# Kernel optimization log

Hardware: AMD Instinct MI355X
Metric: run time of the kernel (lower is better)

Reference implementation:

```python
import jax, jax.numpy as jnp
import numpy as np

RADIUS = 9.0   # search_raduis_scale * particle_radius
K = 20         # N_neighbor
HIDDEN = [512, 512, 512, 512]


def embed(x, n_freqs):
    freqs = 2.0 ** jnp.arange(n_freqs, dtype=x.dtype)      # [F]
    xf = x[..., None, :] * freqs[:, None]                  # [..., F, C]
    sc = jnp.stack([jnp.sin(xf), jnp.cos(xf)], axis=-2)    # [..., F, 2, C]
    return jnp.concatenate([x, sc.reshape(*x.shape[:-1], -1)], axis=-1)


def ball_query(q, p, radius, k):
    # pytorch3d semantics: first k points (by index order) with squared dist < radius^2;
    # padding slots get dists=0, idx=-1, nn=0.
    n = p.shape[0]
    d2 = jnp.sum((q[:, None, :] - p[None, :, :]) ** 2, axis=-1)   # [P,N]
    valid = d2 < radius * radius
    score = jnp.where(valid, -jnp.arange(n, dtype=q.dtype), -jnp.inf)
    top, idx = jax.lax.top_k(score, k)                            # first k valid indices
    found = top > -jnp.inf
    safe = jnp.clip(idx, 0, n - 1)
    dists = jnp.where(found, jnp.take_along_axis(d2, safe, axis=1), 0.0)
    nn = jnp.where(found[..., None], p[safe], 0.0)                # [P,K,3]
    return dists, jnp.where(found, idx, -1), nn


def mlp(x, params):
    n = len(params)
    for l, (v, g, b) in enumerate(params):
        w = g * v / jnp.linalg.norm(v, axis=1, keepdims=True)     # weight_norm, dim=0
        x = x @ w.T + b
        if l < n - 1:
            x = jax.nn.relu(x)
    return jax.nn.sigmoid(x)


def setup_inputs() -> dict:
    key = jax.random.key(0)
    ks = jax.random.split(key, 32)
    R, S, N, F = 256, 128, 4096, 256
    P = R * S
    inp = {
        "points": jax.random.normal(ks[0], (P, 3), dtype=jnp.float32) * 3.0,
        "normals": jax.random.normal(ks[1], (P, 3), dtype=jnp.float32),
        "view_dirs": jax.random.normal(ks[2], (P, 3), dtype=jnp.float32),
        "feature_vectors": jax.random.normal(ks[3], (P, F), dtype=jnp.float32),
        "phys_points": jax.random.normal(ks[4], (N, 3), dtype=jnp.float32) * 3.0,
        "ray_dirs": jax.random.normal(ks[5], (R, 3), dtype=jnp.float32),
        "cam_loc": jax.random.normal(ks[6], (1, 3), dtype=jnp.float32),
    }
    d0 = 3 + 3 + 3 + F + 63 + 9 + 63 + 63 + 27 + 27   # = 517
    dims = [d0] + HIDDEN + [3]
    for l in range(len(dims) - 1):
        fan_in, fan_out = dims[l], dims[l + 1]
        inp[f"v{l}"] = jax.random.normal(ks[7 + l], (fan_out, fan_in), dtype=jnp.float32) * float(np.sqrt(2.0 / fan_out))
        inp[f"g{l}"] = jnp.ones((fan_out, 1), dtype=jnp.float32)
        inp[f"b{l}"] = jnp.zeros((fan_out,), dtype=jnp.float32)
    return inp


def reference(points, normals, view_dirs, feature_vectors, phys_points, ray_dirs, cam_loc,
              v0, g0, b0, v1, g1, b1, v2, g2, b2, v3, g3, b3, v4, g4, b4):
    params = [(v0, g0, b0), (v1, g1, b1), (v2, g2, b2), (v3, g3, b3), (v4, g4, b4)]
    # mode == 'idr'
    rendering_input = jnp.concatenate([points, view_dirs, normals, feature_vectors], axis=-1)
    dists, idx, neighbors = ball_query(points, phys_points, RADIUS, K)
    nn_mask = dists != 0                                             # [P,K]
    num_nn = nn_mask.sum(-1, keepdims=True).astype(points.dtype)     # [P,1]
    # smoothing_position (exclude_ray=True): Euclidean dists recomputed incl. zero-padded slots
    dd = jnp.linalg.norm(neighbors - points[:, None, :], axis=-1)    # [P,K]
    w = jnp.maximum(1.0 - (dd / RADIUS) ** 3, 0.0)
    smoothed_pos = (w[..., None] * neighbors).sum(-2) / (w.sum(-1, keepdims=True) + 1e-12)
    density = w.sum(-1, keepdims=True)                               # [P,1]
    d = smoothed_pos - cam_loc                                       # broadcast [P,3]
    smoothed_dir = d / jnp.linalg.norm(d, axis=-1, keepdims=True)
    # variance of masked neighbor offsets
    vec = jnp.where(nn_mask[..., None], neighbors - points[:, None, :], 0.0)
    vec_mean = vec.sum(-2) / (num_nn + 1e-12)                        # [P,3]
    var = jnp.where(nn_mask[..., None], (vec - vec_mean[:, None, :]) ** 2, 0.0).sum(-2) / (num_nn + 1e-12)
    reps = points.shape[0] // ray_dirs.shape[0]                      # samples per ray
    hit_dir_emb = jnp.repeat(embed(ray_dirs, 4), reps, axis=0)       # [P,27]
    feats = jnp.concatenate([embed(points, 10), embed(density, 4), embed(smoothed_pos, 10),
                             embed(var, 10), hit_dir_emb, embed(smoothed_dir, 4)], axis=-1)
    x = jnp.concatenate([rendering_input, feats], axis=-1)           # [P,517]
    return mlp(x, params)
```

## Files before the change

### kernel.cpp

```cpp
#include <hip/hip_runtime.h>
#include <hip/hip_bf16.h>

typedef unsigned short u16;
typedef short short8 __attribute__((ext_vector_type(8)));
typedef unsigned short ushort8 __attribute__((ext_vector_type(8)));
typedef float f32x4 __attribute__((ext_vector_type(4)));

static __device__ __forceinline__ u16 f2bf(float f) {
  unsigned u = __builtin_bit_cast(unsigned, f);
  unsigned r = (u + 0x7fffu + ((u >> 16) & 1u)) >> 16;
  return (u16)r;
}
static __device__ __forceinline__ float bf2f(u16 h) {
  unsigned u = ((unsigned)h) << 16;
  return __builtin_bit_cast(float, u);
}

static __device__ __forceinline__ void gload_lds16(const u16* g, u16* l) {
  __builtin_amdgcn_global_load_lds(
      (const __attribute__((address_space(1))) void*)g,
      (__attribute__((address_space(3))) void*)l, 16, 0, 0);
}


static __device__ void prep_w0_body(const float* __restrict__ v,
                                    const float* __restrict__ g,
                                    u16* __restrict__ out, int row, int lane) {
  double s = 0.0;
  for (int k = lane; k < 517; k += 64) {
    double x = (double)v[(size_t)row * 517 + k];
    s += x * x;
  }
#pragma unroll
  for (int off = 32; off; off >>= 1) s += __shfl_xor(s, off);
  double scale = (double)g[row] / sqrt(s);

  for (int j = lane; j < 576; j += 64) {
    int orig = -1;
    if (j < 256) {
      orig = 9 + j;
    } else if (j < 281) {
      int e = j - 256;
      if (e < 9)       orig = e;
      else if (e < 12) orig = 265 + (e - 9);
      else if (e == 12) orig = 328;
      else if (e < 16) orig = 337 + (e - 13);
      else if (e < 19) orig = 400 + (e - 16);
      else if (e < 22) orig = 463 + (e - 19);
      else if (e < 25) orig = 490 + (e - 22);
    } else if (j >= 288 && j < 524) {
      int t = j - 288;
      if (t < 60)       orig = 268 + t;
      else if (t < 68)  orig = 329 + (t - 60);
      else if (t < 128) orig = 340 + (t - 68);
      else if (t < 188) orig = 403 + (t - 128);
      else if (t < 212) orig = 466 + (t - 188);
      else if (t < 236) orig = 493 + (t - 212);
    }
    float wv = (orig >= 0) ? (float)((double)v[(size_t)row * 517 + orig] * scale) : 0.0f;
    out[(size_t)row * 576 + j] = f2bf(wv);
  }
}

static __device__ void prep_w_body(const float* __restrict__ v,
                                   const float* __restrict__ g,
                                   u16* __restrict__ out, int row, int lane) {
  double s = 0.0;
  for (int k = lane; k < 512; k += 64) {
    double x = (double)v[(size_t)row * 512 + k];
    s += x * x;
  }
#pragma unroll
  for (int off = 32; off; off >>= 1) s += __shfl_xor(s, off);
  double scale = (double)g[row] / sqrt(s);
  for (int k = lane; k < 512; k += 64)
    out[(size_t)row * 512 + k] = f2bf((float)((double)v[(size_t)row * 512 + k] * scale));
}

static __device__ void prep_w4_body(const float* __restrict__ v,
                                    const float* __restrict__ g,
                                    float* __restrict__ out, int row, int lane) {
  double s = 0.0;
  for (int k = lane; k < 512; k += 64) {
    double x = (double)v[(size_t)row * 512 + k];
    s += x * x;
  }
#pragma unroll
  for (int off = 32; off; off >>= 1) s += __shfl_xor(s, off);
  double scale = (double)g[row] / sqrt(s);
  for (int k = lane; k < 512; k += 64)
    out[(size_t)row * 512 + k] = (float)((double)v[(size_t)row * 512 + k] * scale);
}

static __device__ void build_tb_body(u16* __restrict__ TB, int lane) {
  for (int i = lane; i < 320; i += 64) {
    const int j = 256 + i;
    unsigned d = 0;
    if (j < 281) {
      int e = j - 256;
      int src = -1;
      if (e < 9)       src = e;
      else if (e < 12) src = e - 9;
      else if (e == 12) src = 9;
      else if (e < 16) src = 10 + (e - 13);
      else if (e < 19) src = 13 + (e - 16);
      else if (e < 22) src = 16 + (e - 19);
      else if (e < 25) src = 19 + (e - 22);
      if (src >= 0) d = 1u | ((unsigned)src << 2);
    } else if (j >= 288 && j < 524) {
      int t = j - 288;
      if (t < 236) {
        int base, src0;
        if (t < 60)       { base = 0;   src0 = 0;  }
        else if (t < 68)  { base = 60;  src0 = 9;  }
        else if (t < 128) { base = 68;  src0 = 10; }
        else if (t < 188) { base = 128; src0 = 13; }
        else if (t < 212) { base = 188; src0 = 16; }
        else              { base = 212; src0 = 19; }
        int u = t - base;
        int f, cs, src;
        if (src0 == 9) { f = u >> 1; cs = u & 1; src = 9; }
        else { f = u / 6; int r = u - 6 * f; cs = (r >= 3) ? 1 : 0; src = src0 + (cs ? r - 3 : r); }
        d = 2u | ((unsigned)src << 2) | ((unsigned)cs << 7) | ((unsigned)f << 8);
      }
    }
    TB[i] = (u16)d;
  }
}

__global__ void prep_all(const float* __restrict__ v0, const float* __restrict__ g0,
                         const float* __restrict__ v1, const float* __restrict__ g1,
                         const float* __restrict__ v2, const float* __restrict__ g2,
                         const float* __restrict__ v3, const float* __restrict__ g3,
                         const float* __restrict__ v4, const float* __restrict__ g4,
                         u16* __restrict__ W0, u16* __restrict__ W1,
                         u16* __restrict__ W2, u16* __restrict__ W3,
                         float* __restrict__ W4, u16* __restrict__ TB) {
  const int b = blockIdx.x;
  const int lane = threadIdx.x;
  if (b < 512)       prep_w0_body(v0, g0, W0, b, lane);
  else if (b < 1024) prep_w_body(v1, g1, W1, b - 512, lane);
  else if (b < 1536) prep_w_body(v2, g2, W2, b - 1024, lane);
  else if (b < 2048) prep_w_body(v3, g3, W3, b - 1536, lane);
  else if (b == 2048) {
    for (int r = 0; r < 3; ++r) prep_w4_body(v4, g4, W4, r, lane);
  } else {
    build_tb_body(TB, lane);
  }
}

__global__ __launch_bounds__(256) void scan_kernel(
    const float* __restrict__ pts, const float* __restrict__ phys,
    u16* __restrict__ idxbuf) {
  const int m = (int)((blockIdx.x * blockDim.x + threadIdx.x) >> 6);
  const int lane = (int)(threadIdx.x & 63);

  const double qx = (double)pts[m * 3 + 0];
  const double qy = (double)pts[m * 3 + 1];
  const double qz = (double)pts[m * 3 + 2];

  u16* __restrict__ row = idxbuf + (size_t)m * 24;

  int found = 0;
  for (int base = 0; base < 4096 && found < 20; base += 64) {
    const int j = base + lane;
    const double px = (double)phys[j * 3 + 0];
    const double py = (double)phys[j * 3 + 1];
    const double pz = (double)phys[j * 3 + 2];
    const double dx = px - qx, dy = py - qy, dz = pz - qz;
    const double d2 = dx * dx + dy * dy + dz * dz;
    const bool valid = d2 < 81.0;
    const unsigned long long mb = __ballot(valid);
    const int rank = found + __popcll(mb & ((1ull << lane) - 1ull));
    if (valid && rank < 20) row[rank] = (u16)j;
    found += __popcll(mb);
    if (found > 20) found = 20;
  }
  if (lane == 0) row[20] = (u16)found;
}

__global__ __launch_bounds__(256) void gstats_kernel(
    const float* __restrict__ pts, const float* __restrict__ phys,
    const float* __restrict__ cam, const u16* __restrict__ idxbuf,
    float* __restrict__ Pbuf) {
  const int i = blockIdx.x * 256 + threadIdx.x;

  const double qx = (double)pts[i * 3 + 0];
  const double qy = (double)pts[i * 3 + 1];
  const double qz = (double)pts[i * 3 + 2];

  const u16* __restrict__ row = idxbuf + (size_t)i * 24;
  const int cnt = (int)row[20];

  int nnn = 0;
  double w_sum = 0, wpx = 0, wpy = 0, wpz = 0;
  double Sx = 0, Sy = 0, Sz = 0, Qx = 0, Qy = 0, Qz = 0;

#pragma unroll
  for (int s = 0; s < 20; ++s) {
    if (s < cnt) {
      const int j = (int)row[s];
      const double px = (double)phys[j * 3 + 0];
      const double py = (double)phys[j * 3 + 1];
      const double pz = (double)phys[j * 3 + 2];
      const double dx = px - qx, dy = py - qy, dz = pz - qz;
      const double d2 = dx * dx + dy * dy + dz * dz;
      const float d2f = (float)d2;
      float wf = 1.0f - d2f * sqrtf(d2f) * (1.0f / 729.0f);
      if (wf < 0.0f) wf = 0.0f;
      const double w = (double)wf;
      w_sum += w; wpx += w * px; wpy += w * py; wpz += w * pz;
      if (d2 != 0.0) {
        nnn += 1;
        Sx += dx; Sy += dy; Sz += dz;
        Qx += dx * dx; Qy += dy * dy; Qz += dz * dz;
      }
    }
  }

  {
    const float q2f = (float)(qx * qx + qy * qy + qz * qz);
    float wpad = 1.0f - q2f * sqrtf(q2f) * (1.0f / 729.0f);
    if (wpad < 0.0f) wpad = 0.0f;
    w_sum += (double)(20 - cnt) * (double)wpad;
  }

  const double inv_denom = 1.0 / (w_sum + 1e-12);
  const double sposx = wpx * inv_denom, sposy = wpy * inv_denom, sposz = wpz * inv_denom;

  const double inv_nd = 1.0 / ((double)nnn + 1e-12);
  const double vmx = Sx * inv_nd, vmy = Sy * inv_nd, vmz = Sz * inv_nd;
  const float vax = (float)((Qx - 2.0 * vmx * Sx + (double)nnn * vmx * vmx) * inv_nd);
  const float vay = (float)((Qy - 2.0 * vmy * Sy + (double)nnn * vmy * vmy) * inv_nd);
  const float vaz = (float)((Qz - 2.0 * vmz * Sz + (double)nnn * vmz * vmz) * inv_nd);

  const double ddx = sposx - (double)cam[0];
  const double ddy = sposy - (double)cam[1];
  const double ddz = sposz - (double)cam[2];
  const double inv_dnm = 1.0 / sqrt(ddx * ddx + ddy * ddy + ddz * ddz);

  f32x4* out = (f32x4*)(Pbuf + (size_t)i * 12);
  f32x4 o0, o1, o2;
  o0[0] = (float)w_sum; o0[1] = (float)sposx; o0[2] = (float)sposy; o0[3] = (float)sposz;
  o1[0] = vax; o1[1] = vay; o1[2] = vaz; o1[3] = (float)(ddx * inv_dnm);
  o2[0] = (float)(ddy * inv_dnm); o2[1] = (float)(ddz * inv_dnm); o2[2] = 0.0f; o2[3] = 0.0f;
  out[0] = o0; out[1] = o1; out[2] = o2;
}

__global__ __launch_bounds__(576) void emb_kernel(
    const float* __restrict__ pts, const float* __restrict__ nrm,
    const float* __restrict__ vdir, const float* __restrict__ fv,
    const float* __restrict__ rdir, const float* __restrict__ Pbuf,
    const u16* __restrict__ TB, u16* __restrict__ X) {
  const int cc = (int)threadIdx.x;
  const int y = (int)threadIdx.y;
  const int m = blockIdx.x * 8 + y;

  __shared__ float sc[8][24];
  if (cc < 22) {
    float v;
    if (cc < 3)       v = pts[m * 3 + cc];
    else if (cc < 6)  v = vdir[m * 3 + (cc - 3)];
    else if (cc < 9)  v = nrm[m * 3 + (cc - 6)];
    else if (cc < 10) v = Pbuf[(size_t)m * 12 + 0];
    else if (cc < 13) v = Pbuf[(size_t)m * 12 + 1 + (cc - 10)];
    else if (cc < 16) v = Pbuf[(size_t)m * 12 + 4 + (cc - 13)];
    else if (cc < 19) v = rdir[(m >> 7) * 3 + (cc - 16)];
    else              v = Pbuf[(size_t)m * 12 + 7 + (cc - 19)];
    sc[y][cc] = v;
  }
  __syncthreads();

  u16* __restrict__ xp = X + (size_t)m * 576 + cc * 8;

  if (cc < 32) {
    const f32x4* fp = (const f32x4*)(fv + (size_t)m * 256 + cc * 8);
    f32x4 a = fp[0], b = fp[1];
    short8 o;
    o[0] = (short)f2bf(a[0]); o[1] = (short)f2bf(a[1]);
    o[2] = (short)f2bf(a[2]); o[3] = (short)f2bf(a[3]);
    o[4] = (short)f2bf(b[0]); o[5] = (short)f2bf(b[1]);
    o[6] = (short)f2bf(b[2]); o[7] = (short)f2bf(b[3]);
    *(short8*)xp = o;
  } else {
    ushort8 tb = *(const ushort8*)(TB + (size_t)(cc - 32) * 8);
    short8 o;
#pragma unroll
    for (int e = 0; e < 8; ++e) {
      const unsigned d = (unsigned)tb[e];
      const unsigned kind = d & 3u;
      float val = 0.0f;
      if (kind) {
        float x = sc[y][(d >> 2) & 31u];
        if (kind == 2u) {
          x *= __builtin_bit_cast(float, (127u + (d >> 8)) << 23);
          float r = x * 0.15915494309189535f + (((d >> 7) & 1u) ? 0.25f : 0.0f);
          r -= floorf(r);
          val = __builtin_amdgcn_sinf(r);
        } else {
          val = x;
        }
      }
      o[e] = (short)f2bf(val);
    }
    *(short8*)xp = o;
  }
}

template <int KTILES>
__global__ __launch_bounds__(512, 2) void gemm_relu(const u16* __restrict__ A,
                                                    const u16* __restrict__ B,
                                                    const float* __restrict__ bias,
                                                    u16* __restrict__ C) {
  constexpr int K = KTILES * 64;
  constexpr int EPS = 264;
  __shared__ __align__(16) u16 smem[67584];
#define AS_(b, r) (smem + (size_t)(b) * 32768 + (size_t)(r) * 64)
#define BS_(b, r) (smem + (size_t)(b) * 32768 + 16384 + (size_t)(r) * 64)

  const int t = threadIdx.x;
  const int lane = t & 63;
  const int wid = t >> 6;
  const int wm = wid >> 2;
  const int wn = wid & 3;

  const int bid = blockIdx.x;
  const int wgid = (bid & 7) * 32 + (bid >> 3);
  const int n0 = (wgid & 1) * 256;
  const int m0 = (wgid >> 1) * 256;

  const int srow = lane >> 3;
  const int gcol = ((lane & 7) ^ srow) * 8;

  f32x4 acc[8][4] = {};

#define STAGE(kt, b)                                                           \
  {                                                                            \
    const int k0_ = (kt) * 64;                                                 \
    _Pragma("unroll")                                                          \
    for (int i_ = 0; i_ < 4; ++i_) {                                           \
      const int rbase_ = wid * 8 + i_ * 64;                                    \
      const int row_ = rbase_ + srow;                                          \
      gload_lds16(A + (size_t)(m0 + row_) * K + k0_ + gcol, AS_(b, rbase_));   \
      gload_lds16(B + (size_t)(n0 + row_) * K + k0_ + gcol, BS_(b, rbase_));   \
    }                                                                          \
  }

  STAGE(0, 0);

  const int rsw = lane & 7;
  for (int kt = 0; kt < KTILES; ++kt) {
    const int cur = kt & 1;
    __builtin_amdgcn_s_barrier();
    if (kt + 1 < KTILES) {
      STAGE(kt + 1, cur ^ 1);
      asm volatile("s_waitcnt vmcnt(8)" ::: "memory");
    } else {
      asm volatile("s_waitcnt vmcnt(0)" ::: "memory");
    }
    __builtin_amdgcn_s_barrier();
#pragma unroll
    for (int ks = 0; ks < 2; ++ks) {
      short8 af[8], bfv[4];
      const int fr = lane & 15;
      const int cc = ((ks * 4 + (lane >> 4)) ^ rsw) * 8;
#pragma unroll
      for (int f = 0; f < 8; ++f)
        af[f] = *(const short8*)(AS_(cur, wm * 128 + f * 16 + fr) + cc);
#pragma unroll
      for (int f = 0; f < 4; ++f)
        bfv[f] = *(const short8*)(BS_(cur, wn * 64 + f * 16 + fr) + cc);
#pragma unroll
      for (int fm = 0; fm < 8; ++fm)
#pragma unroll
        for (int fn = 0; fn < 4; ++fn)
          acc[fm][fn] = __builtin_amdgcn_mfma_f32_16x16x32_bf16(af[fm], bfv[fn], acc[fm][fn], 0, 0, 0);
    }
  }
#undef STAGE

  __syncthreads();
  const int lr = lane >> 4, lc = lane & 15;
#pragma unroll
  for (int fn = 0; fn < 4; ++fn) {
    const int tcol = wn * 64 + fn * 16 + lc;
    const float bv = bias[n0 + tcol];
#pragma unroll
    for (int fm = 0; fm < 8; ++fm) {
      const int rowb = wm * 128 + fm * 16 + lr * 4;
#pragma unroll
      for (int rg = 0; rg < 4; ++rg) {
        float vv = fmaxf(acc[fm][fn][rg] + bv, 0.0f);
        smem[(size_t)(rowb + rg) * EPS + tcol] = f2bf(vv);
      }
    }
  }
  __syncthreads();
#pragma unroll
  for (int it = 0; it < 16; ++it) {
    const int row = wid * 32 + it * 2 + (lane >> 5);
    const int ch = lane & 31;
    short8 v = *(const short8*)(smem + (size_t)row * EPS + ch * 8);
    *(short8*)(C + (size_t)(m0 + row) * 512 + n0 + ch * 8) = v;
  }
#undef AS_
#undef BS_
}

__global__ __launch_bounds__(256) void final_kernel(const u16* __restrict__ H,
                                                    const float* __restrict__ W4,
                                                    const float* __restrict__ b4,
                                                    float* __restrict__ out) {
  const int m = (int)((blockIdx.x * blockDim.x + threadIdx.x) >> 6);
  const int lane = (int)(threadIdx.x & 63);

  short8 hv = *(const short8*)(H + (size_t)m * 512 + lane * 8);
  float x[8];
#pragma unroll
  for (int e = 0; e < 8; ++e) x[e] = bf2f((u16)hv[e]);

  float s0 = 0, s1 = 0, s2 = 0;
  const float* w0 = W4 + 0 * 512 + lane * 8;
  const float* w1 = W4 + 1 * 512 + lane * 8;
  const float* w2 = W4 + 2 * 512 + lane * 8;
#pragma unroll
  for (int e = 0; e < 8; ++e) {
    s0 += x[e] * w0[e];
    s1 += x[e] * w1[e];
    s2 += x[e] * w2[e];
  }
#pragma unroll
  for (int off = 32; off; off >>= 1) {
    s0 += __shfl_xor(s0, off);
    s1 += __shfl_xor(s1, off);
    s2 += __shfl_xor(s2, off);
  }
  if (lane < 3) {
    float v = (lane == 0) ? s0 : (lane == 1 ? s1 : s2);
    v += b4[lane];
    out[(size_t)m * 3 + lane] = 1.0f / (1.0f + expf(-v));
  }
}

extern "C" void kernel_launch(void* const* d_in, const int* in_sizes, int n_in,
                              void* d_out, int out_size, void* d_ws, size_t ws_size,
                              hipStream_t stream) {
  const float* pts  = (const float*)d_in[0];
  const float* nrm  = (const float*)d_in[1];
  const float* vdir = (const float*)d_in[2];
  const float* fv   = (const float*)d_in[3];
  const float* phys = (const float*)d_in[4];
  const float* rdir = (const float*)d_in[5];
  const float* cam  = (const float*)d_in[6];
  const float* v0 = (const float*)d_in[7];  const float* g0 = (const float*)d_in[8];  const float* b0 = (const float*)d_in[9];
  const float* v1 = (const float*)d_in[10]; const float* g1 = (const float*)d_in[11]; const float* b1 = (const float*)d_in[12];
  const float* v2 = (const float*)d_in[13]; const float* g2 = (const float*)d_in[14]; const float* b2 = (const float*)d_in[15];
  const float* v3 = (const float*)d_in[16]; const float* g3 = (const float*)d_in[17]; const float* b3 = (const float*)d_in[18];
  const float* v4 = (const float*)d_in[19]; const float* g4 = (const float*)d_in[20]; const float* b4 = (const float*)d_in[21];

  char* ws = (char*)d_ws;
  u16*      W0 = (u16*)(ws + 0);
  u16*      W1 = (u16*)(ws + 589824);
  u16*      W2 = (u16*)(ws + 1114112);
  u16*      W3 = (u16*)(ws + 1638400);
  float*    W4 = (float*)(ws + 2162688);
  u16*      TB = (u16*)(ws + 2168832);
  u16*      Ix = (u16*)(ws + 2171136);
  float*    Pb = (float*)(ws + 3744000);
  u16*      X  = (u16*)(ws + 5316864);
  u16*      H1 = (u16*)(ws + 43065600);
  u16*      H2 = X;

  prep_all<<<2050, 64, 0, stream>>>(v0, g0, v1, g1, v2, g2, v3, g3, v4, g4,
                                    W0, W1, W2, W3, W4, TB);

  scan_kernel<<<8192, 256, 0, stream>>>(pts, phys, Ix);
  gstats_kernel<<<128, 256, 0, stream>>>(pts, phys, cam, Ix, Pb);
  emb_kernel<<<4096, dim3(72, 8), 0, stream>>>(pts, nrm, vdir, fv, rdir, Pb, TB, X);

  gemm_relu<9><<<256, 512, 0, stream>>>(X,  W0, b0, H1);
  gemm_relu<8><<<256, 512, 0, stream>>>(H1, W1, b1, H2);
  gemm_relu<8><<<256, 512, 0, stream>>>(H2, W2, b2, H1);
  gemm_relu<8><<<256, 512, 0, stream>>>(H1, W3, b3, H2);

  final_kernel<<<8192, 256, 0, stream>>>(H2, W4, b4, (float*)d_out);
}
```

Before: 152.6 us.

## Interleave next-tile global-to-LDS loads with MFMA quarters and raise priority

The K-loop of the GEMM kernel now issues the next tile's global-to-LDS loads one slab at a time, each interleaved with a quarter of the MFMA work, instead of issuing all loads up front. It waits only for the current tile's loads, then computes in four chunks of two M-fragments, with B fragments hoisted once per tile. s_setprio is raised around the MFMA bursts. This aims to hide memory latency and LDS reads behind matrix math. In exchange it adds more barriers per tile and keeps more fragments live in registers.

```diff
diff --git a/kernel.cpp b/kernel.cpp
--- a/kernel.cpp
+++ b/kernel.cpp
@@ -334,50 +334,66 @@
 
   f32x4 acc[8][4] = {};
 
-#define STAGE(kt, b)                                                           \
+#define STAGE_SLAB(kt, b, i_)                                                  \
   {                                                                            \
     const int k0_ = (kt) * 64;                                                 \
-    _Pragma("unroll")                                                          \
-    for (int i_ = 0; i_ < 4; ++i_) {                                           \
-      const int rbase_ = wid * 8 + i_ * 64;                                    \
-      const int row_ = rbase_ + srow;                                          \
-      gload_lds16(A + (size_t)(m0 + row_) * K + k0_ + gcol, AS_(b, rbase_));   \
-      gload_lds16(B + (size_t)(n0 + row_) * K + k0_ + gcol, BS_(b, rbase_));   \
-    }                                                                          \
-  }
-
-  STAGE(0, 0);
+    const int rbase_ = wid * 8 + (i_) * 64;                                    \
+    const int row_ = rbase_ + srow;                                            \
+    gload_lds16(A + (size_t)(m0 + row_) * K + k0_ + gcol, AS_(b, rbase_));     \
+    gload_lds16(B + (size_t)(n0 + row_) * K + k0_ + gcol, BS_(b, rbase_));     \
+  }
+
+#pragma unroll
+  for (int i = 0; i < 4; ++i) STAGE_SLAB(0, 0, i);
 
   const int rsw = lane & 7;
+  const int fr = lane & 15;
+  const int hi = lane >> 4;
+
   for (int kt = 0; kt < KTILES; ++kt) {
     const int cur = kt & 1;
-    __builtin_amdgcn_s_barrier();
-    if (kt + 1 < KTILES) {
-      STAGE(kt + 1, cur ^ 1);
-      asm volatile("s_waitcnt vmcnt(8)" ::: "memory");
-    } else {
-      asm volatile("s_waitcnt vmcnt(0)" ::: "memory");
+    const bool has_next = (kt + 1 < KTILES);
+    short8 bfv[4][2];
+#pragma unroll
+    for (int q = 0; q < 4; ++q) {
+      if (has_next) STAGE_SLAB(kt + 1, cur ^ 1, q);
+      if (q == 0) {
+        if (has_next) {
+          asm volatile("s_waitcnt vmcnt(2)" ::: "memory");
+        } else {
+          asm volatile("s_waitcnt vmcnt(0)" ::: "memory");
+        }
+        __builtin_amdgcn_s_barrier();
+#pragma unroll
+        for (int fn = 0; fn < 4; ++fn)
+#pragma unroll
+          for (int ks = 0; ks < 2; ++ks) {
+            const int cc = ((ks * 4 + hi) ^ rsw) * 8;
+            bfv[fn][ks] = *(const short8*)(BS_(cur, wn * 64 + fn * 16 + fr) + cc);
+          }
+      }
+      short8 af[2][2];
+#pragma unroll
+      for (int j = 0; j < 2; ++j)
+#pragma unroll
+        for (int ks = 0; ks < 2; ++ks) {
+          const int cc = ((ks * 4 + hi) ^ rsw) * 8;
+          af[j][ks] = *(const short8*)(AS_(cur, wm * 128 + (2 * q + j) * 16 + fr) + cc);
+        }
+      __builtin_amdgcn_s_setprio(1);
+#pragma unroll
+      for (int j = 0; j < 2; ++j)
+#pragma unroll
+        for (int fn = 0; fn < 4; ++fn)
+#pragma unroll
+          for (int ks = 0; ks < 2; ++ks)
+            acc[2 * q + j][fn] = __builtin_amdgcn_mfma_f32_16x16x32_bf16(
+                af[j][ks], bfv[fn][ks], acc[2 * q + j][fn], 0, 0, 0);
+      __builtin_amdgcn_s_setprio(0);
+      __builtin_amdgcn_s_barrier();
     }
-    __builtin_amdgcn_s_barrier();
-#pragma unroll
-    for (int ks = 0; ks < 2; ++ks) {
-      short8 af[8], bfv[4];
-      const int fr = lane & 15;
-      const int cc = ((ks * 4 + (lane >> 4)) ^ rsw) * 8;
-#pragma unroll
-      for (int f = 0; f < 8; ++f)
-        af[f] = *(const short8*)(AS_(cur, wm * 128 + f * 16 + fr) + cc);
-#pragma unroll
-      for (int f = 0; f < 4; ++f)
-        bfv[f] = *(const short8*)(BS_(cur, wn * 64 + f * 16 + fr) + cc);
-#pragma unroll
-      for (int fm = 0; fm < 8; ++fm)
-#pragma unroll
-        for (int fn = 0; fn < 4; ++fn)
-          acc[fm][fn] = __builtin_amdgcn_mfma_f32_16x16x32_bf16(af[fm], bfv[fn], acc[fm][fn], 0, 0, 0);
-    }
-  }
-#undef STAGE
+  }
+#undef STAGE_SLAB
 
   __syncthreads();
   const int lr = lane >> 4, lc = lane & 15;
```

New measurement: 157.2 us. +3.0%, slower.

## Fuse four MLP layers and output head into one LDS-resident kernel

Applied to the files above, without the earlier changes.

Replaces the four separate GEMM+ReLU launches and the final projection kernel with a single kernel. Each block keeps a 128-row activation tile in swizzled LDS across all layers and writes each layer's output back in place. Weight fragments are streamed directly from global memory into registers, double-buffered per k-step. This removes the global round trips of the 32768x512 intermediate activations and four extra launches. In exchange it uses about 147KB of LDS per block, runs one block per CU, and re-reads every weight matrix from L2 in every block with little latency hiding.

```diff
diff --git a/kernel.cpp b/kernel.cpp
--- a/kernel.cpp
+++ b/kernel.cpp
@@ -307,138 +307,138 @@
   }
 }
 
-template <int KTILES>
-__global__ __launch_bounds__(512, 2) void gemm_relu(const u16* __restrict__ A,
-                                                    const u16* __restrict__ B,
-                                                    const float* __restrict__ bias,
-                                                    u16* __restrict__ C) {
-  constexpr int K = KTILES * 64;
-  constexpr int EPS = 264;
-  __shared__ __align__(16) u16 smem[67584];
-#define AS_(b, r) (smem + (size_t)(b) * 32768 + (size_t)(r) * 64)
-#define BS_(b, r) (smem + (size_t)(b) * 32768 + 16384 + (size_t)(r) * 64)
-
-  const int t = threadIdx.x;
+template <int KL>
+static __device__ __forceinline__ void layer_pass(
+    u16* act, const u16* __restrict__ W, const float* __restrict__ bias,
+    int lane, int wm, int wn) {
+  constexpr int NKS = KL / 32;
+  const int fr = lane & 15;
+  const int hi = lane >> 4;
+  f32x4 acc[4][8] = {};
+
+  const u16* __restrict__ Wb = W + (size_t)(wn * 128 + fr) * KL + hi * 8;
+
+#define LOADB(dst, ks)                                                         \
+  _Pragma("unroll")                                                            \
+  for (int fn_ = 0; fn_ < 8; ++fn_)                                            \
+    dst[fn_] = *(const short8*)(Wb + (size_t)fn_ * 16 * KL + (ks) * 32);
+
+#define COMPUTE(Bregs, ks)                                                     \
+  {                                                                            \
+    short8 af_[4];                                                             \
+    _Pragma("unroll")                                                          \
+    for (int fm_ = 0; fm_ < 4; ++fm_) {                                        \
+      const int row_ = wm * 64 + fm_ * 16 + fr;                                \
+      const int ch_ = (ks) * 4 + hi;                                           \
+      const int slot_ = (ch_ & ~7) | ((ch_ ^ (row_ & 7)) & 7);                 \
+      af_[fm_] = *(const short8*)(act + (size_t)row_ * 576 + slot_ * 8);       \
+    }                                                                          \
+    _Pragma("unroll")                                                          \
+    for (int fm_ = 0; fm_ < 4; ++fm_)                                          \
+      _Pragma("unroll")                                                        \
+      for (int fn_ = 0; fn_ < 8; ++fn_)                                        \
+        acc[fm_][fn_] = __builtin_amdgcn_mfma_f32_16x16x32_bf16(               \
+            af_[fm_], Bregs[fn_], acc[fm_][fn_], 0, 0, 0);                     \
+  }
+
+  short8 B0[8], B1[8];
+  LOADB(B0, 0);
+  for (int ks = 0; ks < NKS; ks += 2) {
+    LOADB(B1, ks + 1);
+    COMPUTE(B0, ks);
+    if (ks + 2 < NKS) LOADB(B0, ks + 2);
+    COMPUTE(B1, ks + 1);
+  }
+#undef LOADB
+#undef COMPUTE
+
+  __syncthreads();
+
+  const int lr = lane >> 4, lc = lane & 15;
+#pragma unroll
+  for (int fn = 0; fn < 8; ++fn) {
+    const int col = wn * 128 + fn * 16 + lc;
+    const float bv = bias[col];
+    const int ch = col >> 3;
+    const int ce = col & 7;
+#pragma unroll
+    for (int fm = 0; fm < 4; ++fm) {
+      const int rowb = wm * 64 + fm * 16 + lr * 4;
+#pragma unroll
+      for (int rg = 0; rg < 4; ++rg) {
+        const int row = rowb + rg;
+        const int slot = (ch & ~7) | ((ch ^ (row & 7)) & 7);
+        float vv = fmaxf(acc[fm][fn][rg] + bv, 0.0f);
+        act[(size_t)row * 576 + slot * 8 + ce] = f2bf(vv);
+      }
+    }
+  }
+
+  __syncthreads();
+}
+
+__global__ __launch_bounds__(512) void fused_mlp(
+    const u16* __restrict__ X,
+    const u16* __restrict__ W0, const float* __restrict__ b0,
+    const u16* __restrict__ W1, const float* __restrict__ b1,
+    const u16* __restrict__ W2, const float* __restrict__ b2,
+    const u16* __restrict__ W3, const float* __restrict__ b3,
+    const float* __restrict__ W4, const float* __restrict__ b4,
+    float* __restrict__ out) {
+  __shared__ __align__(16) u16 act[128 * 576];
+
+  const int t = (int)threadIdx.x;
   const int lane = t & 63;
   const int wid = t >> 6;
   const int wm = wid >> 2;
   const int wn = wid & 3;
-
-  const int bid = blockIdx.x;
-  const int wgid = (bid & 7) * 32 + (bid >> 3);
-  const int n0 = (wgid & 1) * 256;
-  const int m0 = (wgid >> 1) * 256;
-
-  const int srow = lane >> 3;
-  const int gcol = ((lane & 7) ^ srow) * 8;
-
-  f32x4 acc[8][4] = {};
-
-#define STAGE(kt, b)                                                           \
-  {                                                                            \
-    const int k0_ = (kt) * 64;                                                 \
-    _Pragma("unroll")                                                          \
-    for (int i_ = 0; i_ < 4; ++i_) {                                           \
-      const int rbase_ = wid * 8 + i_ * 64;                                    \
-      const int row_ = rbase_ + srow;                                          \
-      gload_lds16(A + (size_t)(m0 + row_) * K + k0_ + gcol, AS_(b, rbase_));   \
-      gload_lds16(B + (size_t)(n0 + row_) * K + k0_ + gcol, BS_(b, rbase_));   \
-    }                                                                          \
-  }
-
-  STAGE(0, 0);
-
-  const int rsw = lane & 7;
-  for (int kt = 0; kt < KTILES; ++kt) {
-    const int cur = kt & 1;
-    __builtin_amdgcn_s_barrier();
-    if (kt + 1 < KTILES) {
-      STAGE(kt + 1, cur ^ 1);
-      asm volatile("s_waitcnt vmcnt(8)" ::: "memory");
-    } else {
-      asm volatile("s_waitcnt vmcnt(0)" ::: "memory");
-    }
-    __builtin_amdgcn_s_barrier();
-#pragma unroll
-    for (int ks = 0; ks < 2; ++ks) {
-      short8 af[8], bfv[4];
-      const int fr = lane & 15;
-      const int cc = ((ks * 4 + (lane >> 4)) ^ rsw) * 8;
-#pragma unroll
-      for (int f = 0; f < 8; ++f)
-        af[f] = *(const short8*)(AS_(cur, wm * 128 + f * 16 + fr) + cc);
-#pragma unroll
-      for (int f = 0; f < 4; ++f)
-        bfv[f] = *(const short8*)(BS_(cur, wn * 64 + f * 16 + fr) + cc);
-#pragma unroll
-      for (int fm = 0; fm < 8; ++fm)
-#pragma unroll
-        for (int fn = 0; fn < 4; ++fn)
-          acc[fm][fn] = __builtin_amdgcn_mfma_f32_16x16x32_bf16(af[fm], bfv[fn], acc[fm][fn], 0, 0, 0);
-    }
-  }
-#undef STAGE
-
+  const int m0 = blockIdx.x * 128;
+
+  {
+    const int base_g = t & ~63;
+#pragma unroll
+    for (int i = 0; i < 18; ++i) {
+      const int gb = i * 512 + base_g;
+      const int d = gb + lane;
+      const int row = d / 72;
+      const int sc = d - row * 72;
+      const int src = (sc & ~7) | ((sc ^ (row & 7)) & 7);
+      gload_lds16(X + (size_t)(m0 + row) * 576 + src * 8, act + (size_t)gb * 8);
+    }
+  }
   __syncthreads();
-  const int lr = lane >> 4, lc = lane & 15;
-#pragma unroll
-  for (int fn = 0; fn < 4; ++fn) {
-    const int tcol = wn * 64 + fn * 16 + lc;
-    const float bv = bias[n0 + tcol];
-#pragma unroll
-    for (int fm = 0; fm < 8; ++fm) {
-      const int rowb = wm * 128 + fm * 16 + lr * 4;
-#pragma unroll
-      for (int rg = 0; rg < 4; ++rg) {
-        float vv = fmaxf(acc[fm][fn][rg] + bv, 0.0f);
-        smem[(size_t)(rowb + rg) * EPS + tcol] = f2bf(vv);
+
+  layer_pass<576>(act, W0, b0, lane, wm, wn);
+  layer_pass<512>(act, W1, b1, lane, wm, wn);
+  layer_pass<512>(act, W2, b2, lane, wm, wn);
+  layer_pass<512>(act, W3, b3, lane, wm, wn);
+
+  {
+    const int row = t >> 2;
+    const int part = t & 3;
+    float s0 = 0.0f, s1 = 0.0f, s2 = 0.0f;
+#pragma unroll
+    for (int j = 0; j < 16; ++j) {
+      const int ch = part * 16 + j;
+      const int slot = (ch & ~7) | ((ch ^ (row & 7)) & 7);
+      short8 v = *(const short8*)(act + (size_t)row * 576 + slot * 8);
+#pragma unroll
+      for (int e = 0; e < 8; ++e) {
+        const float h = bf2f((u16)v[e]);
+        const int col = ch * 8 + e;
+        s0 += h * W4[col];
+        s1 += h * W4[512 + col];
+        s2 += h * W4[1024 + col];
       }
     }
-  }
-  __syncthreads();
-#pragma unroll
-  for (int it = 0; it < 16; ++it) {
-    const int row = wid * 32 + it * 2 + (lane >> 5);
-    const int ch = lane & 31;
-    short8 v = *(const short8*)(smem + (size_t)row * EPS + ch * 8);
-    *(short8*)(C + (size_t)(m0 + row) * 512 + n0 + ch * 8) = v;
-  }
-#undef AS_
-#undef BS_
-}
-
-__global__ __launch_bounds__(256) void final_kernel(const u16* __restrict__ H,
-                                                    const float* __restrict__ W4,
-                                                    const float* __restrict__ b4,
-                                                    float* __restrict__ out) {
-  const int m = (int)((blockIdx.x * blockDim.x + threadIdx.x) >> 6);
-  const int lane = (int)(threadIdx.x & 63);
-
-  short8 hv = *(const short8*)(H + (size_t)m * 512 + lane * 8);
-  float x[8];
-#pragma unroll
-  for (int e = 0; e < 8; ++e) x[e] = bf2f((u16)hv[e]);
-
-  float s0 = 0, s1 = 0, s2 = 0;
-  const float* w0 = W4 + 0 * 512 + lane * 8;
-  const float* w1 = W4 + 1 * 512 + lane * 8;
-  const float* w2 = W4 + 2 * 512 + lane * 8;
-#pragma unroll
-  for (int e = 0; e < 8; ++e) {
-    s0 += x[e] * w0[e];
-    s1 += x[e] * w1[e];
-    s2 += x[e] * w2[e];
-  }
-#pragma unroll
-  for (int off = 32; off; off >>= 1) {
-    s0 += __shfl_xor(s0, off);
-    s1 += __shfl_xor(s1, off);
-    s2 += __shfl_xor(s2, off);
-  }
-  if (lane < 3) {
-    float v = (lane == 0) ? s0 : (lane == 1 ? s1 : s2);
-    v += b4[lane];
-    out[(size_t)m * 3 + lane] = 1.0f / (1.0f + expf(-v));
+    s0 += __shfl_xor(s0, 1); s1 += __shfl_xor(s1, 1); s2 += __shfl_xor(s2, 1);
+    s0 += __shfl_xor(s0, 2); s1 += __shfl_xor(s1, 2); s2 += __shfl_xor(s2, 2);
+    if (part == 0) {
+      float* o = out + (size_t)(m0 + row) * 3;
+      o[0] = 1.0f / (1.0f + expf(-(s0 + b4[0])));
+      o[1] = 1.0f / (1.0f + expf(-(s1 + b4[1])));
+      o[2] = 1.0f / (1.0f + expf(-(s2 + b4[2])));
+    }
   }
 }
 
@@ -468,8 +468,6 @@
   u16*      Ix = (u16*)(ws + 2171136);
   float*    Pb = (float*)(ws + 3744000);
   u16*      X  = (u16*)(ws + 5316864);
-  u16*      H1 = (u16*)(ws + 43065600);
-  u16*      H2 = X;
 
   prep_all<<<2050, 64, 0, stream>>>(v0, g0, v1, g1, v2, g2, v3, g3, v4, g4,
                                     W0, W1, W2, W3, W4, TB);
@@ -478,10 +476,6 @@
   gstats_kernel<<<128, 256, 0, stream>>>(pts, phys, cam, Ix, Pb);
   emb_kernel<<<4096, dim3(72, 8), 0, stream>>>(pts, nrm, vdir, fv, rdir, Pb, TB, X);
 
-  gemm_relu<9><<<256, 512, 0, stream>>>(X,  W0, b0, H1);
-  gemm_relu<8><<<256, 512, 0, stream>>>(H1, W1, b1, H2);
-  gemm_relu<8><<<256, 512, 0, stream>>>(H2, W2, b2, H1);
-  gemm_relu<8><<<256, 512, 0, stream>>>(H1, W3, b3, H2);
-
-  final_kernel<<<8192, 256, 0, stream>>>(H2, W4, b4, (float*)d_out);
-}
+  fused_mlp<<<256, 512, 0, stream>>>(X, W0, b0, W1, b1, W2, b2, W3, b3, W4, b4,
+                                     (float*)d_out);
+}
```

Result: slower. 305.4 us (+100.2%).
